# Kernel optimization log

Hardware: AMD Instinct MI355X
Metric: run time of the kernel (lower is better)

The kernel has to match this reference:

```python
import jax, jax.numpy as jnp
from jax import lax
import numpy as np

KSIZE = 21  # fixed 21x21 depthwise kernel
PAD = 10    # ReflectionPad2d(10)
SIGMA = 2.0


def _gaussian_kernel_21(sigma):
    # Replicates scipy.ndimage.gaussian_filter applied to a 21x21 delta image.
    # radius = int(truncate*sigma + 0.5) with truncate=4.0; for sigma=2 -> 8 <= 10,
    # so the separable Gaussian fits inside the 21x21 window exactly.
    radius = int(4.0 * sigma + 0.5)
    xs = np.arange(-radius, radius + 1, dtype=np.float64)
    phi = np.exp(-0.5 * (xs / sigma) ** 2)
    phi /= phi.sum()
    k2 = np.outer(phi, phi)
    K = np.zeros((KSIZE, KSIZE), dtype=np.float64)
    c = KSIZE // 2
    K[c - radius:c + radius + 1, c - radius:c + radius + 1] = k2
    return K.astype(np.float32)


def setup_inputs() -> dict:
    key = jax.random.key(0)
    x = jax.random.normal(key, (16, 3, 512, 512), dtype=jnp.float32)
    k = _gaussian_kernel_21(SIGMA)
    # depthwise conv weight: (out_ch=3, in_ch/groups=1, 21, 21), same kernel per channel
    W = jnp.broadcast_to(jnp.asarray(k)[None, None], (3, 1, KSIZE, KSIZE))
    return {"x": x, "W": W}


def reference(x, W):
    # ReflectionPad2d(10) then depthwise (groups=3) 21x21 conv, no bias
    xp = jnp.pad(x, ((0, 0), (0, 0), (PAD, PAD), (PAD, PAD)), mode="reflect")
    out = lax.conv_general_dilated(
        xp, W,
        window_strides=(1, 1),
        padding="VALID",
        dimension_numbers=("NCHW", "OIHW", "NCHW"),
        feature_group_count=3,
    )
    return out
```

## Files before the change

### kernel.cpp

```cpp
#include <hip/hip_runtime.h>


constexpr int IMG = 512;
constexpr int KS  = 21;
constexpr int RAD = 10;
constexpr int TX  = 64;
constexpr int TY  = 32;
constexpr int HY  = TY + 2 * RAD;
constexpr int SA_STRIDE = 85;
constexpr int SB_STRIDE = 53;

__global__ __launch_bounds__(256, 5) void gauss2d_sep(const float* __restrict__ x,
                                                      const float* __restrict__ W,
                                                      float* __restrict__ out)
{
    __shared__ float sA[HY * SA_STRIDE];
    __shared__ float sB[TX * SB_STRIDE];
    __shared__ float sPhi[KS];

    const int tid = threadIdx.x;
    const int tx  = blockIdx.x * TX;
    const int ty  = blockIdx.y * TY;
    const int bc  = blockIdx.z;
    const int ch  = bc % 3;

    if (tid < KS) {
        const float* wr = W + ch * (KS * KS) + RAD * KS;
        sPhi[tid] = wr[tid] / sqrtf(wr[RAD]);
    }

    const float* __restrict__ xin = x + (size_t)bc * (IMG * IMG);

    if (tid < 252) {
        const int rg = (tid >= 168) ? 2 : (tid >= 84 ? 1 : 0);
        const int c  = tid - rg * 84;
        int gc = tx + c - RAD;
        gc = (gc < 0) ? -gc : gc;
        gc = (gc >= IMG) ? 2 * IMG - 2 - gc : gc;
        for (int rr = rg; rr < HY; rr += 3) {
            int gr = ty + rr - RAD;
            gr = (gr < 0) ? -gr : gr;
            gr = (gr >= IMG) ? 2 * IMG - 2 - gr : gr;
            sA[rr * SA_STRIDE + c] = xin[gr * IMG + gc];
        }
    }
    __syncthreads();

    float ph[KS];
    #pragma unroll
    for (int j = 0; j < KS; ++j)
        ph[j] = __int_as_float(__builtin_amdgcn_readfirstlane(__float_as_int(sPhi[j])));

    if (tid < HY * 4) {
        const int r  = tid >> 2;
        const int c0 = (tid & 3) << 4;
        const float* arow = &sA[r * SA_STRIDE + c0];
        float win[36];
        #pragma unroll
        for (int k = 0; k < 36; ++k) win[k] = arow[k];
        float acc[16];
        #pragma unroll
        for (int i = 0; i < 16; ++i) {
            float a = ph[0] * win[i];
            #pragma unroll
            for (int j = 1; j < KS; ++j) a += ph[j] * win[i + j];
            acc[i] = a;
        }
        #pragma unroll
        for (int i = 0; i < 16; ++i)
            sB[(c0 + i) * SB_STRIDE + r] = acc[i];
    }
    __syncthreads();

    {
        const int c  = tid & 63;
        const int r0 = (tid >> 6) << 3;
        const float* bcol = &sB[c * SB_STRIDE + r0];
        float win[28];
        #pragma unroll
        for (int k = 0; k < 28; ++k) win[k] = bcol[k];
        float acc[8];
        #pragma unroll
        for (int i = 0; i < 8; ++i) {
            float a = ph[0] * win[i];
            #pragma unroll
            for (int j = 1; j < KS; ++j) a += ph[j] * win[i + j];
            acc[i] = a;
        }
        float* __restrict__ oimg = out + (size_t)bc * (IMG * IMG)
                                 + (size_t)(ty + r0) * IMG + (tx + c);
        #pragma unroll
        for (int i = 0; i < 8; ++i)
            oimg[i * IMG] = acc[i];
    }
}

extern "C" void kernel_launch(void* const* d_in, const int* in_sizes, int n_in,
                              void* d_out, int out_size, void* d_ws, size_t ws_size,
                              hipStream_t stream) {
    const float* x = (const float*)d_in[0];
    const float* W = (const float*)d_in[1];
    float* out     = (float*)d_out;
    dim3 grid(IMG / TX, IMG / TY, 16 * 3);
    gauss2d_sep<<<grid, 256, 0, stream>>>(x, W, out);
}
```

Baseline: 123.4 us.

## Halve tile height, use float4 interior loads and row-major vectorized smem

Reduces the tile height from 32 to 16 rows and raises the occupancy hint from 5 to 7. Interior tiles now load the halo with aligned float4 global loads and no reflection math; only border tiles take the scalar reflected path. The horizontal pass reads and writes shared memory as float4, storing its output row-major instead of transposed. The Gaussian taps are computed per thread from global memory, removing the shared-memory staging. The shorter tile raises the halo overhead (36 input rows per 16 output rows instead of 52 per 32) and gives each thread less vertical work.

After: 149.9 us. 1.21x slower.

```diff
diff --git a/kernel.cpp b/kernel.cpp
--- a/kernel.cpp
+++ b/kernel.cpp
@@ -5,92 +5,100 @@
 constexpr int KS  = 21;
 constexpr int RAD = 10;
 constexpr int TX  = 64;
-constexpr int TY  = 32;
+constexpr int TY  = 16;
 constexpr int HY  = TY + 2 * RAD;
-constexpr int SA_STRIDE = 85;
-constexpr int SB_STRIDE = 53;
+constexpr int SAQ = 23;
+constexpr int SBF = 68;
 
-__global__ __launch_bounds__(256, 5) void gauss2d_sep(const float* __restrict__ x,
+__global__ __launch_bounds__(256, 7) void gauss2d_sep(const float* __restrict__ x,
                                                       const float* __restrict__ W,
                                                       float* __restrict__ out)
 {
-    __shared__ float sA[HY * SA_STRIDE];
-    __shared__ float sB[TX * SB_STRIDE];
-    __shared__ float sPhi[KS];
+    __shared__ float4 sA4[HY * SAQ];
+    __shared__ float4 sB4[HY * (SBF / 4)];
+    float* sA = (float*)sA4;
+    float* sB = (float*)sB4;
 
     const int tid = threadIdx.x;
-    const int tx  = blockIdx.x * TX;
-    const int ty  = blockIdx.y * TY;
-    const int bc  = blockIdx.z;
-    const int ch  = bc % 3;
+    const int bx = blockIdx.x, by = blockIdx.y, bc = blockIdx.z;
+    const int tx = bx * TX, ty = by * TY;
+    const int ch = bc % 3;
 
-    if (tid < KS) {
-        const float* wr = W + ch * (KS * KS) + RAD * KS;
-        sPhi[tid] = wr[tid] / sqrtf(wr[RAD]);
-    }
+    const float* wr = W + ch * (KS * KS) + RAD * KS;
+    const float inv = 1.0f / sqrtf(wr[RAD]);
+    float ph[KS];
+    #pragma unroll
+    for (int j = 0; j < KS; ++j)
+        ph[j] = __int_as_float(__builtin_amdgcn_readfirstlane(__float_as_int(wr[j] * inv)));
 
     const float* __restrict__ xin = x + (size_t)bc * (IMG * IMG);
 
-    if (tid < 252) {
-        const int rg = (tid >= 168) ? 2 : (tid >= 84 ? 1 : 0);
-        const int c  = tid - rg * 84;
-        int gc = tx + c - RAD;
-        gc = (gc < 0) ? -gc : gc;
-        gc = (gc >= IMG) ? 2 * IMG - 2 - gc : gc;
-        for (int rr = rg; rr < HY; rr += 3) {
-            int gr = ty + rr - RAD;
-            gr = (gr < 0) ? -gr : gr;
-            gr = (gr >= IMG) ? 2 * IMG - 2 - gr : gr;
-            sA[rr * SA_STRIDE + c] = xin[gr * IMG + gc];
+    const bool interior = (bx >= 1) & (bx <= 6) & (by >= 1) & (by <= 30);
+    if (interior) {
+        const float4* xin4 = (const float4*)xin;
+        const int base4 = ((ty - RAD) * IMG + (tx - 12)) >> 2;
+        for (int e = tid; e < HY * 22; e += 256) {
+            int r = e / 22, q = e - r * 22;
+            sA4[r * SAQ + q] = xin4[base4 + r * (IMG / 4) + q];
+        }
+    } else {
+        for (int e = tid; e < HY * 88; e += 256) {
+            int r = e / 88, c = e - r * 88;
+            int gr = ty + r - RAD;
+            gr = (gr < 0) ? -gr : gr;  gr = (gr >= IMG) ? 2 * IMG - 2 - gr : gr;
+            int gc = tx + c - 12;
+            gc = (gc < 0) ? -gc : gc;  gc = (gc >= IMG) ? 2 * IMG - 2 - gc : gc;
+            sA[r * (4 * SAQ) + c] = xin[gr * IMG + gc];
         }
     }
     __syncthreads();
 
-    float ph[KS];
-    #pragma unroll
-    for (int j = 0; j < KS; ++j)
-        ph[j] = __int_as_float(__builtin_amdgcn_readfirstlane(__float_as_int(sPhi[j])));
-
-    if (tid < HY * 4) {
-        const int r  = tid >> 2;
-        const int c0 = (tid & 3) << 4;
-        const float* arow = &sA[r * SA_STRIDE + c0];
-        float win[36];
+    for (int e = tid; e < HY * 8; e += 256) {
+        const int r  = e >> 3;
+        const int c0 = (e & 7) << 3;
+        float4 w4[8];
         #pragma unroll
-        for (int k = 0; k < 36; ++k) win[k] = arow[k];
-        float acc[16];
+        for (int k = 0; k < 8; ++k) w4[k] = sA4[r * SAQ + (c0 >> 2) + k];
+        float win[32];
         #pragma unroll
-        for (int i = 0; i < 16; ++i) {
-            float a = ph[0] * win[i];
+        for (int k = 0; k < 8; ++k) {
+            win[4 * k]     = w4[k].x;  win[4 * k + 1] = w4[k].y;
+            win[4 * k + 2] = w4[k].z;  win[4 * k + 3] = w4[k].w;
+        }
+        float acc[8];
+        #pragma unroll
+        for (int i = 0; i < 8; ++i) {
+            float a = ph[0] * win[i + 2];
             #pragma unroll
-            for (int j = 1; j < KS; ++j) a += ph[j] * win[i + j];
+            for (int j = 1; j < KS; ++j) a += ph[j] * win[i + 2 + j];
             acc[i] = a;
         }
-        #pragma unroll
-        for (int i = 0; i < 16; ++i)
-            sB[(c0 + i) * SB_STRIDE + r] = acc[i];
+        float4 o0 = {acc[0], acc[1], acc[2], acc[3]};
+        float4 o1 = {acc[4], acc[5], acc[6], acc[7]};
+        sB4[r * (SBF / 4) + (c0 >> 2)]     = o0;
+        sB4[r * (SBF / 4) + (c0 >> 2) + 1] = o1;
     }
     __syncthreads();
 
     {
-        const int c  = tid & 63;
-        const int r0 = (tid >> 6) << 3;
-        const float* bcol = &sB[c * SB_STRIDE + r0];
-        float win[28];
+        const int c = tid & 63;
+        const int g = tid >> 6;
+        float win[24];
         #pragma unroll
-        for (int k = 0; k < 28; ++k) win[k] = bcol[k];
-        float acc[8];
+        for (int k = 0; k < 24; ++k)
+            win[k] = sB[(4 * g + k) * SBF + c];
+        float acc[4];
         #pragma unroll
-        for (int i = 0; i < 8; ++i) {
+        for (int i = 0; i < 4; ++i) {
             float a = ph[0] * win[i];
             #pragma unroll
             for (int j = 1; j < KS; ++j) a += ph[j] * win[i + j];
             acc[i] = a;
         }
         float* __restrict__ oimg = out + (size_t)bc * (IMG * IMG)
-                                 + (size_t)(ty + r0) * IMG + (tx + c);
+                                 + (size_t)(ty + 4 * g) * IMG + (tx + c);
         #pragma unroll
-        for (int i = 0; i < 8; ++i)
+        for (int i = 0; i < 4; ++i)
             oimg[i * IMG] = acc[i];
     }
 }
```

## Fuse horizontal pass with direct global float4 loads, drop input LDS staging

Applied to the files above, without the earlier changes.

Removes the shared-memory staging tile for the input and the first barrier. The horizontal pass now reads each halo row straight from global memory, using aligned float4 loads for interior blocks and scalar reflected loads at the image edges, and accumulates as the data streams in. Filter weights are read per thread directly from global memory rather than through shared memory, and the occupancy hint is raised from 5 to 8 blocks. This cuts LDS traffic and a sync, at the cost of redundant global/L2 reads of overlapping halo columns across threads and more register pressure.

Measured after the change: 170.0 us. 37.7% more time.

```diff
diff --git a/kernel.cpp b/kernel.cpp
--- a/kernel.cpp
+++ b/kernel.cpp
@@ -7,64 +7,71 @@
 constexpr int TX  = 64;
 constexpr int TY  = 32;
 constexpr int HY  = TY + 2 * RAD;
-constexpr int SA_STRIDE = 85;
 constexpr int SB_STRIDE = 53;
 
-__global__ __launch_bounds__(256, 5) void gauss2d_sep(const float* __restrict__ x,
+__device__ __forceinline__ int reflect512(int i) {
+    i = (i < 0) ? -i : i;
+    return (i >= IMG) ? 2 * IMG - 2 - i : i;
+}
+
+__global__ __launch_bounds__(256, 8) void gauss2d_sep(const float* __restrict__ x,
                                                       const float* __restrict__ W,
                                                       float* __restrict__ out)
 {
-    __shared__ float sA[HY * SA_STRIDE];
     __shared__ float sB[TX * SB_STRIDE];
-    __shared__ float sPhi[KS];
 
     const int tid = threadIdx.x;
-    const int tx  = blockIdx.x * TX;
-    const int ty  = blockIdx.y * TY;
-    const int bc  = blockIdx.z;
-    const int ch  = bc % 3;
+    const int bx = blockIdx.x, by = blockIdx.y, bc = blockIdx.z;
+    const int tx = bx * TX, ty = by * TY;
+    const int ch = bc % 3;
 
-    if (tid < KS) {
-        const float* wr = W + ch * (KS * KS) + RAD * KS;
-        sPhi[tid] = wr[tid] / sqrtf(wr[RAD]);
-    }
-
-    const float* __restrict__ xin = x + (size_t)bc * (IMG * IMG);
-
-    if (tid < 252) {
-        const int rg = (tid >= 168) ? 2 : (tid >= 84 ? 1 : 0);
-        const int c  = tid - rg * 84;
-        int gc = tx + c - RAD;
-        gc = (gc < 0) ? -gc : gc;
-        gc = (gc >= IMG) ? 2 * IMG - 2 - gc : gc;
-        for (int rr = rg; rr < HY; rr += 3) {
-            int gr = ty + rr - RAD;
-            gr = (gr < 0) ? -gr : gr;
-            gr = (gr >= IMG) ? 2 * IMG - 2 - gr : gr;
-            sA[rr * SA_STRIDE + c] = xin[gr * IMG + gc];
-        }
-    }
-    __syncthreads();
-
+    const float* wr = W + ch * (KS * KS) + RAD * KS;
+    const float inv = 1.0f / sqrtf(wr[RAD]);
     float ph[KS];
     #pragma unroll
     for (int j = 0; j < KS; ++j)
-        ph[j] = __int_as_float(__builtin_amdgcn_readfirstlane(__float_as_int(sPhi[j])));
+        ph[j] = __int_as_float(__builtin_amdgcn_readfirstlane(__float_as_int(wr[j] * inv)));
+
+    const float* __restrict__ xin = x + (size_t)bc * (IMG * IMG);
 
     if (tid < HY * 4) {
         const int r  = tid >> 2;
         const int c0 = (tid & 3) << 4;
-        const float* arow = &sA[r * SA_STRIDE + c0];
-        float win[36];
-        #pragma unroll
-        for (int k = 0; k < 36; ++k) win[k] = arow[k];
+        const int gr = reflect512(ty + r - RAD);
+        const float* __restrict__ row = xin + (size_t)gr * IMG;
+
         float acc[16];
         #pragma unroll
-        for (int i = 0; i < 16; ++i) {
-            float a = ph[0] * win[i];
+        for (int i = 0; i < 16; ++i) acc[i] = 0.f;
+
+        if (bx >= 1 && bx <= 6) {
+            const float4* __restrict__ row4 =
+                (const float4*)(row + (tx + c0 - 12));
             #pragma unroll
-            for (int j = 1; j < KS; ++j) a += ph[j] * win[i + j];
-            acc[i] = a;
+            for (int k = 0; k < 10; ++k) {
+                const float4 v = row4[k];
+                const float el[4] = {v.x, v.y, v.z, v.w};
+                #pragma unroll
+                for (int m = 0; m < 4; ++m) {
+                    const int w = 4 * k + m;
+                    #pragma unroll
+                    for (int i = 0; i < 16; ++i) {
+                        const int j = w - 2 - i;
+                        if (j >= 0 && j < KS) acc[i] += ph[j] * el[m];
+                    }
+                }
+            }
+        } else {
+            #pragma unroll
+            for (int w = 0; w < 40; ++w) {
+                const int gc = reflect512(tx + c0 - 12 + w);
+                const float v = row[gc];
+                #pragma unroll
+                for (int i = 0; i < 16; ++i) {
+                    const int j = w - 2 - i;
+                    if (j >= 0 && j < KS) acc[i] += ph[j] * v;
+                }
+            }
         }
         #pragma unroll
         for (int i = 0; i < 16; ++i)
```
